# Kernel optimization log

Hardware: AMD Instinct MI355X
Metric: run time of the kernel (lower is better)

The kernel has to match this reference:

```python
import jax, jax.numpy as jnp
import numpy as np

B, F0, D = 512, 40, 32
SIZES = [200, 200, 200]


def _glorot(key, shape):
    fan_in, fan_out = shape[0], shape[1]
    std = np.sqrt(2.0 / (fan_in + fan_out)).astype(np.float32)
    return jax.random.normal(key, shape, dtype=jnp.float32) * std


def setup_inputs() -> dict:
    key = jax.random.key(0)
    k0, k1, k2, k3 = jax.random.split(key, 4)
    inputs = jax.random.normal(k0, (B, F0, D), dtype=jnp.float32)
    # weights: (field_i * field_0, next_size), matching tf conv1d filter (1, Fi*F0, next)
    W0 = _glorot(k1, (F0 * F0, SIZES[0]))
    W1 = _glorot(k2, (SIZES[0] * F0, SIZES[1]))
    W2 = _glorot(k3, (SIZES[1] * F0, SIZES[2]))
    return {"inputs": inputs, "W0": W0, "W1": W1, "W2": W2}


def _cin(inputs, Ws):
    # inputs: [B, F0, D]; each layer: outer product along field dims per embedding dim,
    # then a 1x1 'conv' (GEMM) mixing the F0*Fi interaction axis down to next size.
    h = inputs
    outs = []
    for W in Ws:
        # z[b,i,j,d] = x0[b,i,d] * h[b,j,d]  -> flatten (i,j) row-major (matches tf reshape)
        z = jnp.einsum('bid,bjd->bijd', inputs, h)
        b, f0, fi, d = z.shape
        z = z.reshape(b, f0 * fi, d)
        # conv1d with kernel width 1 == GEMM over the interaction axis
        h = jnp.einsum('bkd,kn->bnd', z, W)  # [B, next, D]
        outs.append(h)
    out = jnp.concatenate(outs, axis=1)      # [B, sum(sizes), D]
    return jnp.sum(out, axis=-1)             # [B, sum(sizes)]


def reference(inputs, W0, W1, W2):
    return _cin(inputs, [W0, W1, W2])
```

## Files before the change

### kernel.cpp

```cpp
#include <hip/hip_runtime.h>

#define CIN_B 512
#define CIN_F0 40
#define CIN_D 32
#define CIN_S 200

typedef _Float16 f16x8 __attribute__((ext_vector_type(8)));
typedef _Float16 f16x2 __attribute__((ext_vector_type(2)));
typedef float floatx16 __attribute__((ext_vector_type(16)));

__device__ __forceinline__ unsigned short f2h(float f) {
    _Float16 h = (_Float16)f;
    return *(unsigned short*)&h;
}
__device__ __forceinline__ float h2f(unsigned short u) {
    return (float)(*(_Float16*)&u);
}
__device__ __forceinline__ f16x8 mulbc(f16x8 v, unsigned int s2) {
    union { unsigned int u; f16x2 p; } sc; sc.u = s2;
    union { f16x8 h; f16x2 p[4]; } a, r;
    a.h = v;
#pragma unroll
    for (int q = 0; q < 4; ++q) r.p[q] = a.p[q] * sc.p;
    return r.h;
}

template <int FI, int KCPI>
__global__ __launch_bounds__(256) void prep_w(const float* __restrict__ W,
                                              unsigned short* __restrict__ Wtk) {
    const int kc = blockIdx.x;
    const int nn = threadIdx.x;
    const int i = kc / KCPI;
    const int kk = kc - i * KCPI;
    unsigned short v[16];
#pragma unroll
    for (int kw = 0; kw < 16; ++kw) {
        int j = kk * 16 + kw;
        float f = 0.f;
        if (j < FI && nn < CIN_S) f = W[(size_t)(i * FI + j) * CIN_S + nn];
        v[kw] = f2h(f);
    }
    uint4* dst = (uint4*)(Wtk + ((size_t)kc * 256 + nn) * 16);
    dst[0] = ((const uint4*)v)[0];
    dst[1] = ((const uint4*)v)[1];
}

__global__ __launch_bounds__(256) void prep_w2(const float* __restrict__ W,
                                               unsigned short* __restrict__ Wtk) {
    const int kc = blockIdx.x;
    const int nn = threadIdx.x;
    const int i = kc / 13;
    const int kk = kc - i * 13;
    const float sc = (kk == 6) ? 0.5f : 1.0f;
    unsigned short v[16];
#pragma unroll
    for (int kw = 0; kw < 16; ++kw) {
        int j = kk * 16 + kw;
        float f = 0.f;
        if (j < CIN_S && nn < CIN_S) f = sc * W[(size_t)(i * CIN_S + j) * CIN_S + nn];
        v[kw] = f2h(f);
    }
    uint4* dst = (uint4*)(Wtk + ((size_t)kc * 256 + nn) * 16);
    dst[0] = ((const uint4*)v)[0];
    dst[1] = ((const uint4*)v)[1];
}

__global__ __launch_bounds__(256) void prep_w2t(const float* __restrict__ W,
                                                unsigned short* __restrict__ W2t) {
    __shared__ unsigned short T[32][33];
    const int kt = blockIdx.x;
    const int nt = blockIdx.y;
    const int tx = threadIdx.x & 31, ty = threadIdx.x >> 5;
#pragma unroll
    for (int q = 0; q < 4; ++q) {
        int kl = ty + 8 * q;
        int k = kt * 32 + kl, n = nt * 32 + tx;
        float f = (k < 8000 && n < CIN_S) ? W[(size_t)k * CIN_S + n] : 0.f;
        T[kl][tx] = f2h(f);
    }
    __syncthreads();
#pragma unroll
    for (int q = 0; q < 4; ++q) {
        int nl = ty + 8 * q;
        W2t[(size_t)(nt * 32 + nl) * 8192 + kt * 32 + tx] = T[tx][nl];
    }
}

__global__ __launch_bounds__(256) void prep_x(const float* __restrict__ X,
                                              unsigned short* __restrict__ X0hd,
                                              unsigned short* __restrict__ Xh) {
    int e = blockIdx.x * 256 + threadIdx.x;
    int d = e & 31;
    int rest = e >> 5;
    int i = rest % CIN_F0;
    int b = rest / CIN_F0;
    unsigned short v = f2h(X[e]);
    Xh[e] = v;
    X0hd[((size_t)b * CIN_D + d) * 48 + i] = v;
    if (e < CIN_B * CIN_D * 8) {
        int q = e & 7, dd = (e >> 3) & 31, bb = e >> 8;
        X0hd[((size_t)bb * CIN_D + dd) * 48 + 40 + q] = 0;
    }
}

template <int NKC, int KCPI_TOT, int JROW, int MODE, int NB, int WPS>
__global__ __launch_bounds__(448, WPS)
void cin_layer(const unsigned short* __restrict__ Hsrc,
               const unsigned short* __restrict__ Xh,
               const unsigned short* __restrict__ Wtk,
               unsigned short* __restrict__ Hout,
               float* __restrict__ outp) {
    __shared__ __align__(16) unsigned short Bp[NB * NKC * 512];
    __shared__ unsigned int Xl[CIN_F0 * CIN_D];

    const int tid = threadIdx.x;
    const int b0 = blockIdx.x * NB;
    const int jh = (MODE == 1) ? 0 : blockIdx.y;
    const int kks = jh * 6;

    for (int e = tid; e < CIN_F0 * CIN_D; e += 448) {
        unsigned int lo = Xh[(size_t)b0 * (CIN_F0 * CIN_D) + e];
        unsigned int hi = (NB == 2) ? (unsigned int)Xh[(size_t)(b0 + 1) * (CIN_F0 * CIN_D) + e] : 0u;
        Xl[e] = lo | (hi << 16);
    }
    {
        const int j0 = (MODE == 1) ? 0 : jh * 96;
        uint4* Bpu = (uint4*)Bp;
        for (int g = tid; g < NB * 64 * NKC; g += 448) {
            int bb = g / (64 * NKC), r = g - bb * (64 * NKC);
            int d = r / (2 * NKC), c = r - d * (2 * NKC);
            uint4 v = ((const uint4*)Hsrc)[(((size_t)(b0 + bb) * CIN_D + d) * JROW + j0) / 8 + c];
            Bpu[(bb * NKC + (c >> 1)) * 64 + (c & 1) * 32 + d] = v;
        }
    }
    __syncthreads();

    const int wave = tid >> 6, lane = tid & 63;
    const int l32 = lane & 31, hl = lane >> 5;
    const int tile = wave;

    const int aB = (tile * 32 + l32) * 16 + hl * 8;
    constexpr int NS = 20 * NKC;

    f16x8 Ar[2][2];
    f16x8 Br[2][NB];

    auto ldA = [&](int s, int slot) {
        int ss = (s < NS) ? s : (NS - 1);
        int iA = 2 * (ss / NKC), kk = ss % NKC;
        int e = (iA * KCPI_TOT + kks + kk) * 4096 + aB;
        Ar[slot][0] = *(const f16x8*)(Wtk + e);
        Ar[slot][1] = *(const f16x8*)(Wtk + e + KCPI_TOT * 4096);
    };
    auto ldB = [&](int s, int slot) {
        int ss = (s < NS) ? s : (NS - 1);
        int kk = ss % NKC;
        Br[slot][0] = *(const f16x8*)&Bp[(0 * NKC + kk) * 512 + lane * 8];
        if constexpr (NB == 2)
            Br[slot][1] = *(const f16x8*)&Bp[(1 * NKC + kk) * 512 + lane * 8];
    };

    ldA(0, 0);
    ldA(1, 1);
    ldB(0, 0);

    floatx16 acc0, acc1;
#pragma unroll
    for (int r = 0; r < 16; ++r) acc0[r] = 0.f;
    if constexpr (NB == 2) {
#pragma unroll
        for (int r = 0; r < 16; ++r) acc1[r] = 0.f;
    }
    unsigned int xs0a = 0, xs1a = 0, xs0b = 0, xs1b = 0;

#pragma unroll 1
    for (int s0 = 0; s0 < NS; s0 += 2 * NKC) {
#pragma unroll
        for (int t = 0; t < 2 * NKC; ++t) {
            const int s = s0 + t;
            const int kk = t % NKC;
            if (kk == 0) {
                const int iA = (s0 / NKC + (t ? 1 : 0)) * 2;
                unsigned int xpa = Xl[iA * CIN_D + l32];
                unsigned int xpb = Xl[(iA + 1) * CIN_D + l32];
                xs0a = (xpa & 0xffffu) | (xpa << 16);
                xs0b = (xpb & 0xffffu) | (xpb << 16);
                if constexpr (NB == 2) {
                    xs1a = (xpa >> 16) | (xpa & 0xffff0000u);
                    xs1b = (xpb >> 16) | (xpb & 0xffff0000u);
                }
            }
            ldB(s + 1, (t + 1) & 1);
            const int sl = t & 1;
            acc0 = __builtin_amdgcn_mfma_f32_32x32x16_f16(
                Ar[sl][0], mulbc(Br[sl][0], xs0a), acc0, 0, 0, 0);
            if constexpr (NB == 2)
                acc1 = __builtin_amdgcn_mfma_f32_32x32x16_f16(
                    Ar[sl][0], mulbc(Br[sl][1], xs1a), acc1, 0, 0, 0);
            acc0 = __builtin_amdgcn_mfma_f32_32x32x16_f16(
                Ar[sl][1], mulbc(Br[sl][0], xs0b), acc0, 0, 0, 0);
            if constexpr (NB == 2)
                acc1 = __builtin_amdgcn_mfma_f32_32x32x16_f16(
                    Ar[sl][1], mulbc(Br[sl][1], xs1b), acc1, 0, 0, 0);
            ldA(s + 2, sl);
        }
    }

#pragma unroll
    for (int bb = 0; bb < NB; ++bb) {
        const floatx16& a = bb ? acc1 : acc0;

        if constexpr (MODE == 1) {
            unsigned short* dst =
                Hout + ((size_t)(b0 + bb) * CIN_D + l32) * 224 + tile * 32;
#pragma unroll
            for (int qd = 0; qd < 4; ++qd) {
                ushort4 pk;
                pk.x = f2h(a[4 * qd + 0]);
                pk.y = f2h(a[4 * qd + 1]);
                pk.z = f2h(a[4 * qd + 2]);
                pk.w = f2h(a[4 * qd + 3]);
                *(ushort4*)&dst[8 * qd + 4 * hl] = pk;
            }
        }
        if constexpr (MODE == 2) {
            unsigned short* hb2 =
                Hout + (((size_t)jh * CIN_B + b0 + bb) * 208) * CIN_D + l32;
#pragma unroll
            for (int r = 0; r < 16; ++r) {
                int n = tile * 32 + (r & 3) + 8 * (r >> 2) + 4 * hl;
                if (n < 208) hb2[(size_t)n * CIN_D] = f2h(a[r]);
            }
        }

#pragma unroll
        for (int r = 0; r < 16; ++r) {
            float v = a[r];
            v += __shfl_xor(v, 1);
            v += __shfl_xor(v, 2);
            v += __shfl_xor(v, 4);
            v += __shfl_xor(v, 8);
            v += __shfl_xor(v, 16);
            if (l32 == 0) {
                int n = tile * 32 + (r & 3) + 8 * (r >> 2) + 4 * hl;
                if (n < CIN_S) {
                    if constexpr (MODE == 1)
                        outp[(size_t)(b0 + bb) * (3 * CIN_S) + n] = v;
                    else
                        outp[((size_t)jh * CIN_B + b0 + bb) * CIN_S + n] = v;
                }
            }
        }
    }
}

__global__ __launch_bounds__(448) void cin_g(const unsigned short* __restrict__ Xh,
                                             const unsigned short* __restrict__ Hacc,
                                             unsigned short* __restrict__ G) {
    const int b = blockIdx.x;
    const int wave = threadIdx.x >> 6, lane = threadIdx.x & 63;
    const int l32 = lane & 31, hl = lane >> 5;
    const int jt = wave;

    if (wave == 0 && lane < 24) {
        uint4 z; z.x = z.y = z.z = z.w = 0;
        ((uint4*)(G + (size_t)b * 8192 + 8000))[lane] = z;
    }

    f16x8 zed;
#pragma unroll
    for (int q = 0; q < 8; ++q) zed[q] = (_Float16)0.f;

    f16x8 a[2][2];
#pragma unroll
    for (int it = 0; it < 2; ++it) {
        int i = it * 32 + l32;
#pragma unroll
        for (int kh = 0; kh < 2; ++kh)
            a[it][kh] = (i < CIN_F0)
                ? *(const f16x8*)&Xh[((size_t)b * CIN_F0 + i) * CIN_D + kh * 16 + hl * 8]
                : zed;
    }

    const int j = jt * 32 + l32;
    const unsigned short* p0 = Hacc + ((size_t)b * 208 + j) * CIN_D;
    const unsigned short* p1 = Hacc + ((size_t)(CIN_B + b) * 208 + j) * CIN_D;
    f16x8 bf[2];
#pragma unroll
    for (int kh = 0; kh < 2; ++kh)
        bf[kh] = (j < 208)
            ? (*(const f16x8*)(p0 + kh * 16 + hl * 8) +
               *(const f16x8*)(p1 + kh * 16 + hl * 8))
            : zed;

#pragma unroll
    for (int it = 0; it < 2; ++it) {
        floatx16 acc;
#pragma unroll
        for (int r = 0; r < 16; ++r) acc[r] = 0.f;
        acc = __builtin_amdgcn_mfma_f32_32x32x16_f16(a[it][0], bf[0], acc, 0, 0, 0);
        acc = __builtin_amdgcn_mfma_f32_32x32x16_f16(a[it][1], bf[1], acc, 0, 0, 0);
#pragma unroll
        for (int r = 0; r < 16; ++r) {
            int row = (r & 3) + 8 * (r >> 2) + 4 * hl;
            int i = it * 32 + row, jj = jt * 32 + l32;
            if (i < CIN_F0 && jj < CIN_S)
                G[(size_t)b * 8192 + i * CIN_S + jj] = f2h(acc[r]);
        }
    }
}

__global__ __launch_bounds__(64) void cin_l3(const unsigned short* __restrict__ W2t,
                                             const unsigned short* __restrict__ G,
                                             float* __restrict__ outp3) {
    const int mt = blockIdx.x;
    const int bt = blockIdx.y;
    const int kch = blockIdx.z;
    const int lane = threadIdx.x, l32 = lane & 31, hl = lane >> 5;

    const unsigned short* pa = W2t + (size_t)(mt * 32 + l32) * 8192 + kch * 512 + hl * 8;
    const unsigned short* pb = G   + (size_t)(bt * 32 + l32) * 8192 + kch * 512 + hl * 8;

    floatx16 acc;
#pragma unroll
    for (int r = 0; r < 16; ++r) acc[r] = 0.f;

    f16x8 Aa[2], Bb[2];
    Aa[0] = *(const f16x8*)(pa);       Bb[0] = *(const f16x8*)(pb);
    Aa[1] = *(const f16x8*)(pa + 16);  Bb[1] = *(const f16x8*)(pb + 16);

#pragma unroll 1
    for (int s0 = 0; s0 < 32; s0 += 2) {
#pragma unroll
        for (int t = 0; t < 2; ++t) {
            acc = __builtin_amdgcn_mfma_f32_32x32x16_f16(Aa[t], Bb[t], acc, 0, 0, 0);
            Aa[t] = *(const f16x8*)(pa + (s0 + t + 2) * 16);
            Bb[t] = *(const f16x8*)(pb + (s0 + t + 2) * 16);
        }
    }

#pragma unroll
    for (int r = 0; r < 16; ++r) {
        int n = mt * 32 + (r & 3) + 8 * (r >> 2) + 4 * hl;
        if (n < CIN_S)
            outp3[((size_t)kch * CIN_B + bt * 32 + l32) * CIN_S + n] = acc[r];
    }
}

__global__ __launch_bounds__(256) void cin_outc(const float* __restrict__ p2,
                                                const float* __restrict__ p3,
                                                float* __restrict__ out) {
    int e = blockIdx.x * 256 + threadIdx.x;
    int b = e / 400, t = e - b * 400;
    int half = t / 200, n = t - half * 200;
    float s;
    if (half == 0) {
        s = p2[(size_t)b * CIN_S + n] + p2[(size_t)(CIN_B + b) * CIN_S + n];
    } else {
        s = 0.f;
#pragma unroll
        for (int q = 0; q < 16; ++q)
            s += p3[((size_t)q * CIN_B + b) * CIN_S + n];
    }
    out[(size_t)b * 600 + 200 + half * 200 + n] = s;
}

extern "C" void kernel_launch(void* const* d_in, const int* in_sizes, int n_in,
                              void* d_out, int out_size, void* d_ws, size_t ws_size,
                              hipStream_t stream) {
    const float* X  = (const float*)d_in[0];
    const float* W0 = (const float*)d_in[1];
    const float* W1 = (const float*)d_in[2];
    const float* W2 = (const float*)d_in[3];
    float* out = (float*)d_out;

    unsigned short* Wtk1 = (unsigned short*)d_ws;
    unsigned short* Wtk2 = Wtk1 + (size_t)120 * 4096;
    unsigned short* W2t  = Wtk2 + (size_t)520 * 4096;
    unsigned short* X0hd = W2t + (size_t)224 * 8192;
    unsigned short* Xh   = X0hd + (size_t)CIN_B * CIN_D * 48;
    unsigned short* H1   = Xh + (size_t)CIN_B * CIN_F0 * CIN_D;
    unsigned short* Hacc = H1 + (size_t)CIN_B * CIN_D * 224;
    unsigned short* H2n  = Hacc + (size_t)2 * CIN_B * 208 * CIN_D;
    float* outp2 = (float*)(H2n + (size_t)CIN_B * 208 * CIN_D);
    float* outp3 = outp2 + (size_t)2 * CIN_B * CIN_S;
    unsigned short* G = (unsigned short*)(outp3 + (size_t)16 * CIN_B * CIN_S);

    prep_w<CIN_F0, 3><<<120, 256, 0, stream>>>(W0, Wtk1);
    prep_w2<<<520, 256, 0, stream>>>(W1, Wtk2);
    prep_w2t<<<dim3(256, 7), 256, 0, stream>>>(W2, W2t);
    prep_x<<<(CIN_B * CIN_F0 * CIN_D) / 256, 256, 0, stream>>>(X, X0hd, Xh);

    cin_layer<3, 3, 48, 1, 2, 4><<<dim3(CIN_B / 2, 1), 448, 0, stream>>>(
        X0hd, Xh, Wtk1, H1, out);
    cin_layer<7, 13, 224, 2, 2, 4><<<dim3(CIN_B / 2, 2), 448, 0, stream>>>(
        H1, Xh, Wtk2, Hacc, outp2);

    cin_g<<<CIN_B, 448, 0, stream>>>(Xh, Hacc, G);
    cin_l3<<<dim3(7, 16, 16), 64, 0, stream>>>(W2t, G, outp3);

    cin_outc<<<(CIN_B * 400) / 256, 256, 0, stream>>>(outp2, outp3, out);
}
```

Before: 220.2 us.

## Merge prep kernels into one launch and replace final reduction with atomics

Folds the four preprocessing kernels into a single block-indexed prep kernel that also zeroes the layer-2/3 output region. Layer 2 and layer 3 now accumulate their split-K partial sums directly into the output with atomicAdd, so the separate combine kernel and the partial buffers are gone. This cuts three launches plus one kernel's worth of partial-buffer traffic. In exchange it adds atomic contention (16-way on the layer-3 outputs) and makes floating-point summation order nondeterministic.

```diff
diff --git a/kernel.cpp b/kernel.cpp
--- a/kernel.cpp
+++ b/kernel.cpp
@@ -25,81 +25,78 @@
     return r.h;
 }
 
-template <int FI, int KCPI>
-__global__ __launch_bounds__(256) void prep_w(const float* __restrict__ W,
-                                              unsigned short* __restrict__ Wtk) {
-    const int kc = blockIdx.x;
-    const int nn = threadIdx.x;
-    const int i = kc / KCPI;
-    const int kk = kc - i * KCPI;
-    unsigned short v[16];
-#pragma unroll
-    for (int kw = 0; kw < 16; ++kw) {
-        int j = kk * 16 + kw;
-        float f = 0.f;
-        if (j < FI && nn < CIN_S) f = W[(size_t)(i * FI + j) * CIN_S + nn];
-        v[kw] = f2h(f);
-    }
-    uint4* dst = (uint4*)(Wtk + ((size_t)kc * 256 + nn) * 16);
-    dst[0] = ((const uint4*)v)[0];
-    dst[1] = ((const uint4*)v)[1];
-}
-
-__global__ __launch_bounds__(256) void prep_w2(const float* __restrict__ W,
-                                               unsigned short* __restrict__ Wtk) {
-    const int kc = blockIdx.x;
-    const int nn = threadIdx.x;
-    const int i = kc / 13;
-    const int kk = kc - i * 13;
-    const float sc = (kk == 6) ? 0.5f : 1.0f;
-    unsigned short v[16];
-#pragma unroll
-    for (int kw = 0; kw < 16; ++kw) {
-        int j = kk * 16 + kw;
-        float f = 0.f;
-        if (j < CIN_S && nn < CIN_S) f = sc * W[(size_t)(i * CIN_S + j) * CIN_S + nn];
-        v[kw] = f2h(f);
-    }
-    uint4* dst = (uint4*)(Wtk + ((size_t)kc * 256 + nn) * 16);
-    dst[0] = ((const uint4*)v)[0];
-    dst[1] = ((const uint4*)v)[1];
-}
-
-__global__ __launch_bounds__(256) void prep_w2t(const float* __restrict__ W,
-                                                unsigned short* __restrict__ W2t) {
+__global__ __launch_bounds__(256) void prep_all(
+    const float* __restrict__ X,  const float* __restrict__ W0,
+    const float* __restrict__ W1, const float* __restrict__ W2,
+    unsigned short* __restrict__ Wtk1, unsigned short* __restrict__ Wtk2,
+    unsigned short* __restrict__ W2t,  unsigned short* __restrict__ X0hd,
+    unsigned short* __restrict__ Xh,   float* __restrict__ out) {
     __shared__ unsigned short T[32][33];
-    const int kt = blockIdx.x;
-    const int nt = blockIdx.y;
-    const int tx = threadIdx.x & 31, ty = threadIdx.x >> 5;
-#pragma unroll
-    for (int q = 0; q < 4; ++q) {
-        int kl = ty + 8 * q;
-        int k = kt * 32 + kl, n = nt * 32 + tx;
-        float f = (k < 8000 && n < CIN_S) ? W[(size_t)k * CIN_S + n] : 0.f;
-        T[kl][tx] = f2h(f);
-    }
-    __syncthreads();
-#pragma unroll
-    for (int q = 0; q < 4; ++q) {
-        int nl = ty + 8 * q;
-        W2t[(size_t)(nt * 32 + nl) * 8192 + kt * 32 + tx] = T[tx][nl];
-    }
-}
-
-__global__ __launch_bounds__(256) void prep_x(const float* __restrict__ X,
-                                              unsigned short* __restrict__ X0hd,
-                                              unsigned short* __restrict__ Xh) {
-    int e = blockIdx.x * 256 + threadIdx.x;
-    int d = e & 31;
-    int rest = e >> 5;
-    int i = rest % CIN_F0;
-    int b = rest / CIN_F0;
-    unsigned short v = f2h(X[e]);
-    Xh[e] = v;
-    X0hd[((size_t)b * CIN_D + d) * 48 + i] = v;
-    if (e < CIN_B * CIN_D * 8) {
-        int q = e & 7, dd = (e >> 3) & 31, bb = e >> 8;
-        X0hd[((size_t)bb * CIN_D + dd) * 48 + 40 + q] = 0;
+    const int bid = blockIdx.x;
+
+    if (bid < 120) {
+        const int kc = bid, nn = threadIdx.x;
+        const int i = kc / 3, kk = kc - i * 3;
+        unsigned short v[16];
+#pragma unroll
+        for (int kw = 0; kw < 16; ++kw) {
+            int j = kk * 16 + kw;
+            float f = 0.f;
+            if (j < CIN_F0 && nn < CIN_S) f = W0[(size_t)(i * CIN_F0 + j) * CIN_S + nn];
+            v[kw] = f2h(f);
+        }
+        uint4* dst = (uint4*)(Wtk1 + ((size_t)kc * 256 + nn) * 16);
+        dst[0] = ((const uint4*)v)[0];
+        dst[1] = ((const uint4*)v)[1];
+    } else if (bid < 640) {
+        const int kc = bid - 120, nn = threadIdx.x;
+        const int i = kc / 13, kk = kc - i * 13;
+        const float sc = (kk == 6) ? 0.5f : 1.0f;
+        unsigned short v[16];
+#pragma unroll
+        for (int kw = 0; kw < 16; ++kw) {
+            int j = kk * 16 + kw;
+            float f = 0.f;
+            if (j < CIN_S && nn < CIN_S) f = sc * W1[(size_t)(i * CIN_S + j) * CIN_S + nn];
+            v[kw] = f2h(f);
+        }
+        uint4* dst = (uint4*)(Wtk2 + ((size_t)kc * 256 + nn) * 16);
+        dst[0] = ((const uint4*)v)[0];
+        dst[1] = ((const uint4*)v)[1];
+    } else if (bid < 2432) {
+        const int q0 = bid - 640;
+        const int kt = q0 & 255, nt = q0 >> 8;
+        const int tx = threadIdx.x & 31, ty = threadIdx.x >> 5;
+#pragma unroll
+        for (int q = 0; q < 4; ++q) {
+            int kl = ty + 8 * q;
+            int k = kt * 32 + kl, n = nt * 32 + tx;
+            float f = (k < 8000 && n < CIN_S) ? W2[(size_t)k * CIN_S + n] : 0.f;
+            T[kl][tx] = f2h(f);
+        }
+        __syncthreads();
+#pragma unroll
+        for (int q = 0; q < 4; ++q) {
+            int nl = ty + 8 * q;
+            W2t[(size_t)(nt * 32 + nl) * 8192 + kt * 32 + tx] = T[tx][nl];
+        }
+    } else if (bid < 4992) {
+        int e = (bid - 2432) * 256 + threadIdx.x;
+        int d = e & 31;
+        int rest = e >> 5;
+        int i = rest % CIN_F0;
+        int b = rest / CIN_F0;
+        unsigned short v = f2h(X[e]);
+        Xh[e] = v;
+        X0hd[((size_t)b * CIN_D + d) * 48 + i] = v;
+        if (e < CIN_B * CIN_D * 8) {
+            int q = e & 7, dd = (e >> 3) & 31, bb = e >> 8;
+            X0hd[((size_t)bb * CIN_D + dd) * 48 + 40 + q] = 0;
+        }
+    } else {
+        int g = (bid - 4992) * 256 + threadIdx.x;
+        int b = g / 400, t = g - b * 400;
+        out[(size_t)b * 600 + 200 + t] = 0.f;
     }
 }
 
@@ -245,9 +242,9 @@
                 int n = tile * 32 + (r & 3) + 8 * (r >> 2) + 4 * hl;
                 if (n < CIN_S) {
                     if constexpr (MODE == 1)
-                        outp[(size_t)(b0 + bb) * (3 * CIN_S) + n] = v;
+                        outp[(size_t)(b0 + bb) * 600 + n] = v;
                     else
-                        outp[((size_t)jh * CIN_B + b0 + bb) * CIN_S + n] = v;
+                        atomicAdd(&outp[(size_t)(b0 + bb) * 600 + 200 + n], v);
                 }
             }
         }
@@ -312,7 +309,7 @@
 
 __global__ __launch_bounds__(64) void cin_l3(const unsigned short* __restrict__ W2t,
                                              const unsigned short* __restrict__ G,
-                                             float* __restrict__ outp3) {
+                                             float* __restrict__ out) {
     const int mt = blockIdx.x;
     const int bt = blockIdx.y;
     const int kch = blockIdx.z;
@@ -343,26 +340,8 @@
     for (int r = 0; r < 16; ++r) {
         int n = mt * 32 + (r & 3) + 8 * (r >> 2) + 4 * hl;
         if (n < CIN_S)
-            outp3[((size_t)kch * CIN_B + bt * 32 + l32) * CIN_S + n] = acc[r];
-    }
-}
-
-__global__ __launch_bounds__(256) void cin_outc(const float* __restrict__ p2,
-                                                const float* __restrict__ p3,
-                                                float* __restrict__ out) {
-    int e = blockIdx.x * 256 + threadIdx.x;
-    int b = e / 400, t = e - b * 400;
-    int half = t / 200, n = t - half * 200;
-    float s;
-    if (half == 0) {
-        s = p2[(size_t)b * CIN_S + n] + p2[(size_t)(CIN_B + b) * CIN_S + n];
-    } else {
-        s = 0.f;
-#pragma unroll
-        for (int q = 0; q < 16; ++q)
-            s += p3[((size_t)q * CIN_B + b) * CIN_S + n];
-    }
-    out[(size_t)b * 600 + 200 + half * 200 + n] = s;
+            atomicAdd(&out[(size_t)(bt * 32 + l32) * 600 + 400 + n], acc[r]);
+    }
 }
 
 extern "C" void kernel_launch(void* const* d_in, const int* in_sizes, int n_in,
@@ -380,24 +359,16 @@
     unsigned short* X0hd = W2t + (size_t)224 * 8192;
     unsigned short* Xh   = X0hd + (size_t)CIN_B * CIN_D * 48;
     unsigned short* H1   = Xh + (size_t)CIN_B * CIN_F0 * CIN_D;
-    unsigned short* Hacc = H1 + (size_t)CIN_B * CIN_D * 224;
-    unsigned short* H2n  = Hacc + (size_t)2 * CIN_B * 208 * CIN_D;
-    float* outp2 = (float*)(H2n + (size_t)CIN_B * 208 * CIN_D);
-    float* outp3 = outp2 + (size_t)2 * CIN_B * CIN_S;
-    unsigned short* G = (unsigned short*)(outp3 + (size_t)16 * CIN_B * CIN_S);
-
-    prep_w<CIN_F0, 3><<<120, 256, 0, stream>>>(W0, Wtk1);
-    prep_w2<<<520, 256, 0, stream>>>(W1, Wtk2);
-    prep_w2t<<<dim3(256, 7), 256, 0, stream>>>(W2, W2t);
-    prep_x<<<(CIN_B * CIN_F0 * CIN_D) / 256, 256, 0, stream>>>(X, X0hd, Xh);
+    unsigned short* G    = H1 + (size_t)CIN_B * CIN_D * 224;
+    unsigned short* Hacc = G + (size_t)CIN_B * 8192;
+
+    prep_all<<<5792, 256, 0, stream>>>(X, W0, W1, W2, Wtk1, Wtk2, W2t, X0hd, Xh, out);
 
     cin_layer<3, 3, 48, 1, 2, 4><<<dim3(CIN_B / 2, 1), 448, 0, stream>>>(
         X0hd, Xh, Wtk1, H1, out);
     cin_layer<7, 13, 224, 2, 2, 4><<<dim3(CIN_B / 2, 2), 448, 0, stream>>>(
-        H1, Xh, Wtk2, Hacc, outp2);
+        H1, Xh, Wtk2, Hacc, out);
 
     cin_g<<<CIN_B, 448, 0, stream>>>(Xh, Hacc, G);
-    cin_l3<<<dim3(7, 16, 16), 64, 0, stream>>>(W2t, G, outp3);
-
-    cin_outc<<<(CIN_B * 400) / 256, 256, 0, stream>>>(outp2, outp3, out);
-}
+    cin_l3<<<dim3(7, 16, 16), 64, 0, stream>>>(W2t, G, out);
+}
```

New measurement: 271.3 us. 23.2% more time.
